# Optimization experiments

Hardware: AMD Instinct MI355X
Metric: run time of the kernel (lower is better)

Reference implementation:

```python
import jax, jax.numpy as jnp
import numpy as np


def lstm(x, W, U, b):
    """Keras LSTM with activation='relu', recurrent_activation='sigmoid'.
    x: [B, S, E]; W: [E, 4u]; U: [u, 4u]; b: [4u]. Gate order i,f,c,o.
    Returns (all hidden states [B,S,u], last hidden [B,u])."""
    B = x.shape[0]
    u = U.shape[0]
    h0 = jnp.zeros((B, u), x.dtype)
    c0 = jnp.zeros((B, u), x.dtype)

    def step(carry, xt):
        h, c = carry
        z = xt @ W + h @ U + b
        i, f, g, o = jnp.split(z, 4, axis=-1)
        i = jax.nn.sigmoid(i)
        f = jax.nn.sigmoid(f)
        g = jax.nn.relu(g)          # candidate activation = relu
        o = jax.nn.sigmoid(o)
        c = f * c + i * g
        h = o * jax.nn.relu(c)      # output activation = relu
        return (h, c), h

    (hT, _), hs = jax.lax.scan(step, (h0, c0), jnp.swapaxes(x, 0, 1))
    return jnp.swapaxes(hs, 0, 1), hT


def setup_inputs() -> dict:
    key = jax.random.key(0)
    ks = iter(jax.random.split(key, 64))

    def W(*s):
        return jax.random.normal(next(ks), s, jnp.float32) * 0.05

    V = 32000
    inp = {
        "t": jax.random.randint(next(ks), (8, 16, 64), 0, V, jnp.int32),
        "p": jax.random.randint(next(ks), (8, 16, 512), 0, V, jnp.int32),
        "emb_t": W(V, 128),
        "emb_p": W(V, 256),
        # title LSTMs: 128 (return_seq) -> 64
        "tl0_W": W(128, 512), "tl0_U": W(128, 512), "tl0_b": jnp.zeros((512,), jnp.float32),
        "tl1_W": W(128, 256), "tl1_U": W(64, 256),  "tl1_b": jnp.zeros((256,), jnp.float32),
        # title dense: 128 relu, 64 relu, 32 linear
        "td0_W": W(64, 128),  "td0_b": jnp.zeros((128,), jnp.float32),
        "td1_W": W(128, 64),  "td1_b": jnp.zeros((64,), jnp.float32),
        "td2_W": W(64, 32),   "td2_b": jnp.zeros((32,), jnp.float32),
        # parag LSTMs: 256 (rs) -> 128 (rs) -> 64
        "pl0_W": W(256, 1024), "pl0_U": W(256, 1024), "pl0_b": jnp.zeros((1024,), jnp.float32),
        "pl1_W": W(256, 512),  "pl1_U": W(128, 512),  "pl1_b": jnp.zeros((512,), jnp.float32),
        "pl2_W": W(128, 256),  "pl2_U": W(64, 256),   "pl2_b": jnp.zeros((256,), jnp.float32),
        # parag dense: 128 relu, 64 relu, 32 linear
        "pd0_W": W(64, 128),  "pd0_b": jnp.zeros((128,), jnp.float32),
        "pd1_W": W(128, 64),  "pd1_b": jnp.zeros((64,), jnp.float32),
        "pd2_W": W(64, 32),   "pd2_b": jnp.zeros((32,), jnp.float32),
        # head: 256 relu, 128 relu, 64 relu, 32 sigmoid
        "L0_W": W(64, 256),  "L0_b": jnp.zeros((256,), jnp.float32),
        "L1_W": W(256, 128), "L1_b": jnp.zeros((128,), jnp.float32),
        "L2_W": W(128, 64),  "L2_b": jnp.zeros((64,), jnp.float32),
        "L3_W": W(64, 32),   "L3_b": jnp.zeros((32,), jnp.float32),
    }
    return inp


def reference(t, p, emb_t, emb_p,
              tl0_W, tl0_U, tl0_b, tl1_W, tl1_U, tl1_b,
              td0_W, td0_b, td1_W, td1_b, td2_W, td2_b,
              pl0_W, pl0_U, pl0_b, pl1_W, pl1_U, pl1_b, pl2_W, pl2_U, pl2_b,
              pd0_W, pd0_b, pd1_W, pd1_b, pd2_W, pd2_b,
              L0_W, L0_b, L1_W, L1_b, L2_W, L2_b, L3_W, L3_b):
    B, N, St = t.shape
    Sp = p.shape[2]

    # The original loops over B and map_fn over a singleton axis; the math is
    # identical to running the stacks on a flattened [B*N] recurrent batch.
    xt = emb_t[t.reshape(B * N, St)]              # [BN, St, 128]
    xt, _ = lstm(xt, tl0_W, tl0_U, tl0_b)         # [BN, St, 128]
    _, ht = lstm(xt, tl1_W, tl1_U, tl1_b)         # [BN, 64]
    ht = jax.nn.relu(ht @ td0_W + td0_b)
    ht = jax.nn.relu(ht @ td1_W + td1_b)
    ht = ht @ td2_W + td2_b                       # [BN, 32] (no activation)

    xp = emb_p[p.reshape(B * N, Sp)]              # [BN, Sp, 256]
    xp, _ = lstm(xp, pl0_W, pl0_U, pl0_b)
    xp, _ = lstm(xp, pl1_W, pl1_U, pl1_b)
    _, hp = lstm(xp, pl2_W, pl2_U, pl2_b)         # [BN, 64]
    hp = jax.nn.relu(hp @ pd0_W + pd0_b)
    hp = jax.nn.relu(hp @ pd1_W + pd1_b)
    hp = hp @ pd2_W + pd2_b                       # [BN, 32]

    feat = jnp.concatenate([ht, hp], axis=-1).reshape(B, N, 64)
    x = feat.mean(axis=1)                         # reduce_mean over axis=-2 (N)
    x = jax.nn.relu(x @ L0_W + L0_b)
    x = jax.nn.relu(x @ L1_W + L1_b)
    x = jax.nn.relu(x @ L2_W + L2_b)
    x = jax.nn.sigmoid(x @ L3_W + L3_b)           # [B, 32]
    return x
```

## Files before the change

### kernel.cpp

```cpp
#include <hip/hip_runtime.h>
#include <hip/hip_fp16.h>

typedef _Float16 f16;
typedef _Float16 f16x8 __attribute__((ext_vector_type(8)));
typedef float    f32x4 __attribute__((ext_vector_type(4)));
typedef unsigned short ushort;
typedef unsigned int uint;
typedef unsigned long long u64;

__device__ __forceinline__ float sigm(float x) { return 1.f / (1.f + __expf(-x)); }
__device__ __forceinline__ float reluf(float x) { return x > 0.f ? x : 0.f; }
__device__ __forceinline__ float h2f(ushort u) { return (float)__builtin_bit_cast(f16, u); }
__device__ __forceinline__ ushort f2h(float v) { return __builtin_bit_cast(ushort, (f16)v); }

#define LDRLX(p)    __hip_atomic_load((p), __ATOMIC_RELAXED, __HIP_MEMORY_SCOPE_AGENT)
#define STRLX(p, v) __hip_atomic_store((p), (v), __ATOMIC_RELAXED, __HIP_MEMORY_SCOPE_AGENT)
#define MFMA16(a, b, c) __builtin_amdgcn_mfma_f32_16x16x32_f16((a), (b), (c), 0, 0, 0)
#define LBAR() do { asm volatile("s_waitcnt lgkmcnt(0)" ::: "memory"); \
                    __builtin_amdgcn_s_barrier(); } while (0)

__device__ __forceinline__ void poll_all(uint* p, uint need, bool act) {
  bool done = !act;
  while (true) {
    if (!done) done = (LDRLX(p) >= need);
    if (__all((int)done)) break;
    __builtin_amdgcn_s_sleep(1);
  }
}

__device__ __forceinline__ u64 ldr64(const u64* p) {
  return __hip_atomic_load(p, __ATOMIC_RELAXED, __HIP_MEMORY_SCOPE_AGENT);
}
__device__ __forceinline__ void str64(u64* p, u64 v) {
  __hip_atomic_store(p, v, __ATOMIC_RELAXED, __HIP_MEMORY_SCOPE_AGENT);
}

template <int NR>
__device__ __forceinline__ void poll_recs(const u64* const (&ra)[NR],
                                          const uint (&nd)[NR], u64 (&rv)[NR]) {
  bool ok[NR];
#pragma unroll
  for (int i = 0; i < NR; i++) ok[i] = (nd[i] == 0u);
  while (true) {
    bool all = true;
#pragma unroll
    for (int i = 0; i < NR; i++) if (!ok[i]) rv[i] = ldr64(ra[i]);
#pragma unroll
    for (int i = 0; i < NR; i++) if (!ok[i]) ok[i] = ((uint)(rv[i] >> 32) >= nd[i]);
#pragma unroll
    for (int i = 0; i < NR; i++) all &= ok[i];
    if (all) return;
    __builtin_amdgcn_s_sleep(1);
  }
}

template <int KF>
__global__ void pack_bsw(const float* __restrict__ B, f16* __restrict__ dst, int N) {
  int id = blockIdx.x * 256 + threadIdx.x;
  int total = KF * 32 * N;
  if (id >= total) return;
  int j  = id & 7;
  int L  = (id >> 3) & 63;
  int r  = id >> 9;
  int kf = r & (KF - 1);
  int c  = r / KF;
  int k  = kf * 32 + ((L >> 4) * 8) + j;
  int n  = c * 16 + (L & 15);
  dst[id] = (f16)B[k * N + n];
}

template <int Sx, int K, int KF, int N, int NC, int MODE>
__global__ __launch_bounds__(256) void gemm_xw(const int* __restrict__ tok,
                                               const float* __restrict__ emb,
                                               const f16* __restrict__ Bsw,
                                               const float* __restrict__ bias,
                                               f16* __restrict__ X) {
  __shared__ int tokLds[64];
  __shared__ f16x8 bLds[8 * 64];
  const int tid = threadIdx.x;
  const int blk = blockIdx.x;
  const int g  = (MODE == 0) ? (blk >> 7) : (blk >> 4);
  const int t0 = (MODE == 0) ? ((blk & 127) * 4) : ((blk & 15) * 4);
  if (tid < 64) {
    int wv = tid >> 4, rho = tid & 15;
    tokLds[tid] = tok[(g * 16 + rho) * Sx + t0 + wv];
  }
  __syncthreads();
  const int wave = tid >> 6, lane = tid & 63;
  const int quad = lane >> 4, l16 = lane & 15;

  f16x8 a[KF];
  {
    const float* arow = emb + (long)tokLds[wave * 16 + l16] * K + quad * 8;
#pragma unroll
    for (int kf = 0; kf < KF; kf++) {
      float4 v0 = *(const float4*)(arow + kf * 32);
      float4 v1 = *(const float4*)(arow + kf * 32 + 4);
      f16x8 tv;
      tv[0] = (f16)v0.x; tv[1] = (f16)v0.y; tv[2] = (f16)v0.z; tv[3] = (f16)v0.w;
      tv[4] = (f16)v1.x; tv[5] = (f16)v1.y; tv[6] = (f16)v1.z; tv[7] = (f16)v1.w;
      a[kf] = tv;
    }
  }
  const int t = t0 + wave;
  const f16x8* Bfrag = (const f16x8*)Bsw;
  for (int c = 0; c < NC; c++) {
    for (int i = tid; i < KF * 64; i += 256) bLds[i] = Bfrag[c * KF * 64 + i];
    __syncthreads();
    f32x4 acc = {0.f, 0.f, 0.f, 0.f};
#pragma unroll
    for (int kf = 0; kf < KF; kf++)
      acc = MFMA16(a[kf], bLds[kf * 64 + lane], acc);
    const int col = c * 16 + l16;
    const float bc = bias[col];
    uint2 pk;
    pk.x = (uint)f2h(acc[0] + bc) | ((uint)f2h(acc[1] + bc) << 16);
    pk.y = (uint)f2h(acc[2] + bc) | ((uint)f2h(acc[3] + bc) << 16);
    size_t base;
    if (MODE == 0) {
      int gm = col >> 8, u = col & 255;
      base = (((size_t)(g * 512 + t) * 4 + gm) * 4096) + u * 16 + quad * 4;
    } else {
      int gm = col >> 7, u = col & 127;
      base = (((size_t)(g * 64 + t) * 4 + gm) * 2048) + u * 16 + quad * 4;
    }
    *(uint2*)(X + base) = pk;
    __syncthreads();
  }
}

struct RP {
  const f16 *xp2, *xt2;
  const f16 *U0f, *W1f, *U1f, *W2f, *U2f, *U0tf, *W1tf, *U1tf;
  const float *pl1_b, *pl2_b, *tl1_b;
  const float *pd0W, *pd0b, *pd1W, *pd1b, *pd2W, *pd2b;
  const float *td0W, *td0b, *td1W, *td1b, *td2W, *td2b;
  u64 *h0r, *h1r, *h0tr;
  uint *cnt;
  float* feat;
};

__global__ __launch_bounds__(256, 1) void recur_pipe(RP A) {
  __shared__ __align__(16) char smem[147968];
  const int tid = threadIdx.x;
  const int w = tid >> 6, lane = tid & 63;
  const int quad = lane >> 4, l16 = lane & 15;
  const int blk = blockIdx.x;
  const int role = blk >> 3, g = blk & 7;
  uint* mytag = A.cnt + (role * 8 + g) * 16;

  if (role < 4) {
    const int bb = role;
    f16* wlds = (f16*)smem;
    f16* hb   = (f16*)(smem + 131072);
    {
      const uint4* U0q = (const uint4*)A.U0f;
      uint4* wq = (uint4*)wlds;
      for (int idx = tid; idx < 8192; idx += 256) {
        int gm = idx >> 11, r = idx & 2047, wv = r >> 9, kf = (r >> 6) & 7, ln = r & 63;
        wq[idx] = U0q[((gm * 16 + 4 * bb + wv) * 8 + kf) * 64 + ln];
      }
    }
    for (int idx = tid; idx < 4224; idx += 256) hb[idx] = (f16)0.f;
    float c0[4] = {0.f, 0.f, 0.f, 0.f};
    u64* ringg = A.h0r + (size_t)g * 16384;
    int pp[3]; { int q = 0; for (int p = 0; p < 4; p++) if (p != bb) pp[q++] = p; }
    const uint2* xq2 = (const uint2*)A.xp2;
    const f16x8* wv8 = (const f16x8*)wlds;
    const int myu = 64 * bb + 16 * w + l16;
    const int ulq = 16 * ((tid >> 4) & 3) + (tid & 15);
    const int qd  = tid >> 6;
    uint* bpp = A.cnt;
    if (lane < 4) bpp = A.cnt + ((4 + lane) * 8 + g) * 16;
    __syncthreads();

    for (int t = 0; t < 512; t++) {
      uint2 xv[4];
      {
        size_t xb = ((size_t)(g * 512 + t) * 4) * 1024 + (size_t)myu * 4 + quad;
#pragma unroll
        for (int gm = 0; gm < 4; gm++) xv[gm] = xq2[xb + (size_t)gm * 1024];
      }
      {
        bool act = (lane < 4) && (t > 0) && ((t & 3) == 0);
        uint need = t > 4 ? (uint)(t - 4) : 0u;
        poll_all(bpp, need, act);
      }
      {
        const u64* slotb = ringg + (size_t)((t + 7) & 7) * 2048;
        const u64* ra[6]; uint nd[6]; u64 rv[6];
#pragma unroll
        for (int q = 0; q < 3; q++) {
          const u64* rb = slotb + pp[q] * 512 + 2 * tid;
          ra[q * 2] = rb; ra[q * 2 + 1] = rb + 1;
          nd[q * 2] = nd[q * 2 + 1] = (t > 0) ? (uint)t : 0u;
        }
        poll_recs<6>(ra, nd, rv);
        if (t > 0) {
          f16* dst = hb + (t & 1) * 4224;
#pragma unroll
          for (int q = 0; q < 3; q++)
#pragma unroll
            for (int j = 0; j < 2; j++) {
              uint pay = (uint)rv[q * 2 + j];
              int r0 = qd * 4 + 2 * j;
              dst[r0 * 264 + pp[q] * 64 + ulq]       = __builtin_bit_cast(f16, (ushort)pay);
              dst[(r0 + 1) * 264 + pp[q] * 64 + ulq] = __builtin_bit_cast(f16, (ushort)(pay >> 16));
            }
        }
      }
      LBAR();
      f16x8 af[8];
#pragma unroll
      for (int kf = 0; kf < 8; kf++)
        af[kf] = *(const f16x8*)&hb[(t & 1) * 4224 + l16 * 264 + kf * 32 + quad * 8];
      f32x4 z[4];
#pragma unroll
      for (int gm = 0; gm < 4; gm++) {
        f32x4 zz = {0.f, 0.f, 0.f, 0.f};
#pragma unroll
        for (int kf = 0; kf < 8; kf++)
          zz = MFMA16(af[kf], wv8[((gm * 4 + w) * 8 + kf) * 64 + lane], zz);
        z[gm] = zz;
      }
      u64 xs[4];
#pragma unroll
      for (int gm = 0; gm < 4; gm++) xs[gm] = ((u64)xv[gm].y << 32) | xv[gm].x;
      ushort hs[4];
      f16* wbuf = hb + ((t + 1) & 1) * 4224;
#pragma unroll
      for (int r = 0; r < 4; r++) {
        float gi = sigm(z[0][r] + h2f((ushort)(xs[0] >> (16 * r))));
        float ff = sigm(z[1][r] + h2f((ushort)(xs[1] >> (16 * r))));
        float gg = reluf(z[2][r] + h2f((ushort)(xs[2] >> (16 * r))));
        float oo = sigm(z[3][r] + h2f((ushort)(xs[3] >> (16 * r))));
        c0[r] = ff * c0[r] + gi * gg;
        hs[r] = f2h(oo * reluf(c0[r]));
        wbuf[(quad * 4 + r) * 264 + myu] = __builtin_bit_cast(f16, hs[r]);
      }
      {
        u64 tg = ((u64)(uint)(t + 1)) << 32;
        u64* wb = ringg + (size_t)(t & 7) * 2048 + bb * 512 +
                  quad * 128 + w * 32 + l16 * 2;
        str64(wb,     tg | (u64)((uint)hs[0] | ((uint)hs[1] << 16)));
        str64(wb + 1, tg | (u64)((uint)hs[2] | ((uint)hs[3] << 16)));
      }
    }
  } else if (role < 8) {
    const int bn = role - 4;
    f16* wlds = (f16*)smem;
    f16* h0c  = (f16*)(smem + 98304);
    f16* h1b  = (f16*)(smem + 106752);
    float* zL = (float*)(smem + 115456);
    {
      const uint4* W1q = (const uint4*)A.W1f;
      const uint4* U1q = (const uint4*)A.U1f;
      uint4* wq = (uint4*)wlds;
      for (int idx = tid; idx < 4096; idx += 256) {
        int gm = idx >> 10, r = idx & 1023, j2 = r >> 9, kf = (r >> 6) & 7, ln = r & 63;
        wq[idx] = W1q[((gm * 8 + bn * 2 + j2) * 8 + kf) * 64 + ln];
      }
      for (int idx = tid; idx < 2048; idx += 256) {
        int gm = idx >> 9, r = idx & 511, j2 = r >> 8, kf = (r >> 6) & 3, ln = r & 63;
        wq[4096 + idx] = U1q[((gm * 8 + bn * 2 + j2) * 4 + kf) * 64 + ln];
      }
    }
    for (int idx = tid; idx < 2176; idx += 256) h1b[idx] = (f16)0.f;
    float c1[2] = {0.f, 0.f};
    float bth[4];
    { int un = tid & 31; for (int gm = 0; gm < 4; gm++) bth[gm] = A.pl1_b[gm * 128 + 32 * bn + un]; }
    u64* h0rg = A.h0r + (size_t)g * 16384;
    u64* h1rg = A.h1r + (size_t)g * 8192;
    int pp[3]; { int q = 0; for (int p = 0; p < 4; p++) if (p != bn) pp[q++] = p; }
    const f16x8* wv8 = (const f16x8*)wlds;
    uint* bpp = A.cnt + (8 * 8 + g) * 16;
    __syncthreads();

    for (int t = 0; t < 512; t++) {
      {
        bool act = (lane == 0) && ((t & 3) == 0);
        uint need = t > 4 ? (uint)(t - 4) : 0u;
        poll_all(bpp, need, act);
      }
      const u64* ra[11]; uint nd[11]; u64 rv[11];
      {
        const u64* s0b = h0rg + (size_t)(t & 7) * 2048;
#pragma unroll
        for (int e = 0; e < 8; e++) { ra[e] = s0b + tid + 256 * e; nd[e] = (uint)(t + 1); }
        const u64* s1b = h1rg + (size_t)((t + 7) & 7) * 1024;
#pragma unroll
        for (int q = 0; q < 3; q++) { ra[8 + q] = s1b + pp[q] * 256 + tid; nd[8 + q] = (t > 0) ? (uint)t : 0u; }
      }
      poll_recs<11>(ra, nd, rv);
      {
#pragma unroll
        for (int e = 0; e < 8; e++) {
          int idx = tid + 256 * e;
          int bbq = idx >> 9, r = idx & 511;
          int jj = r & 1, l16c = (r >> 1) & 15, wc = (r >> 5) & 3, qdc = (r >> 7) & 3;
          int col = bbq * 64 + 16 * wc + l16c;
          int r0 = qdc * 4 + 2 * jj;
          uint pay = (uint)rv[e];
          h0c[r0 * 264 + col]       = __builtin_bit_cast(f16, (ushort)pay);
          h0c[(r0 + 1) * 264 + col] = __builtin_bit_cast(f16, (ushort)(pay >> 16));
        }
        if (t > 0) {
          f16* dst = h1b + (t & 1) * 2176;
          int sqc = tid >> 5, unc = tid & 31;
#pragma unroll
          for (int q = 0; q < 3; q++) {
            uint pay = (uint)rv[8 + q];
            dst[sqc * 136 + pp[q] * 32 + unc]       = __builtin_bit_cast(f16, (ushort)pay);
            dst[(sqc + 8) * 136 + pp[q] * 32 + unc] = __builtin_bit_cast(f16, (ushort)(pay >> 16));
          }
        }
      }
      LBAR();
      if (tid == 0) STRLX(mytag, (uint)(t + 1));
      f16x8 af0[8], af1[4];
#pragma unroll
      for (int kf = 0; kf < 8; kf++)
        af0[kf] = *(const f16x8*)&h0c[l16 * 264 + kf * 32 + quad * 8];
#pragma unroll
      for (int kf = 0; kf < 4; kf++)
        af1[kf] = *(const f16x8*)&h1b[(t & 1) * 2176 + l16 * 136 + kf * 32 + quad * 8];
#pragma unroll
      for (int j2 = 0; j2 < 2; j2++) {
        f32x4 zz = {0.f, 0.f, 0.f, 0.f};
#pragma unroll
        for (int kf = 0; kf < 8; kf++)
          zz = MFMA16(af0[kf], wv8[((w * 2 + j2) * 8 + kf) * 64 + lane], zz);
#pragma unroll
        for (int kf = 0; kf < 4; kf++)
          zz = MFMA16(af1[kf], wv8[4096 + ((w * 2 + j2) * 4 + kf) * 64 + lane], zz);
#pragma unroll
        for (int r = 0; r < 4; r++)
          zL[(quad * 4 + r) * 132 + w * 32 + j2 * 16 + l16] = zz[r];
      }
      LBAR();
      {
        int sq = tid >> 5, un = tid & 31;
        f16* dst = h1b + ((t + 1) & 1) * 2176;
        ushort hh[2];
#pragma unroll
        for (int e = 0; e < 2; e++) {
          int s = sq + 8 * e;
          float gi = sigm(zL[s * 132 + un] + bth[0]);
          float ff = sigm(zL[s * 132 + 32 + un] + bth[1]);
          float gg = reluf(zL[s * 132 + 64 + un] + bth[2]);
          float oo = sigm(zL[s * 132 + 96 + un] + bth[3]);
          c1[e] = ff * c1[e] + gi * gg;
          float hv = oo * reluf(c1[e]);
          hh[e] = f2h(hv);
          dst[s * 136 + 32 * bn + un] = __builtin_bit_cast(f16, hh[e]);
        }
        u64 tg = ((u64)(uint)(t + 1)) << 32;
        str64(h1rg + (size_t)(t & 7) * 1024 + bn * 256 + tid,
              tg | (u64)((uint)hh[0] | ((uint)hh[1] << 16)));
      }
      LBAR();
    }
  } else if (role == 8) {
    f16* wlds = (f16*)smem;
    f16* h1c  = (f16*)(smem + 98304);
    f16* h2db = (f16*)(smem + 107008);
    {
      const uint4* W2q = (const uint4*)A.W2f;
      const uint4* U2q = (const uint4*)A.U2f;
      uint4* wq = (uint4*)wlds;
      for (int idx = tid; idx < 4096; idx += 256) wq[idx] = W2q[idx];
      for (int idx = tid; idx < 2048; idx += 256) wq[4096 + idx] = U2q[idx];
    }
    for (int idx = tid; idx < 1152; idx += 256) h2db[idx] = (f16)0.f;
    float c2[4] = {0.f, 0.f, 0.f, 0.f};
    float b2[4];
#pragma unroll
    for (int gm = 0; gm < 4; gm++) b2[gm] = A.pl2_b[gm * 64 + 16 * w + l16];
    u64* h1rg = A.h1r + (size_t)g * 8192;
    const f16x8* wv8 = (const f16x8*)wlds;
    __syncthreads();

    for (int t = 0; t < 512; t++) {
      const u64* ra[4]; uint nd[4]; u64 rv[4];
      {
        const u64* s1b = h1rg + (size_t)(t & 7) * 1024;
#pragma unroll
        for (int e = 0; e < 4; e++) { ra[e] = s1b + tid + 256 * e; nd[e] = (uint)(t + 1); }
      }
      poll_recs<4>(ra, nd, rv);
      {
        f16* dst = h1c + (t & 1) * 2176;
#pragma unroll
        for (int e = 0; e < 4; e++) {
          int idx = tid + 256 * e;
          int bq = idx >> 8, r = idx & 255;
          int sqc = r >> 5, unc = r & 31;
          uint pay = (uint)rv[e];
          dst[sqc * 136 + bq * 32 + unc]       = __builtin_bit_cast(f16, (ushort)pay);
          dst[(sqc + 8) * 136 + bq * 32 + unc] = __builtin_bit_cast(f16, (ushort)(pay >> 16));
        }
      }
      LBAR();
      if (tid == 0) STRLX(mytag, (uint)(t + 1));
      f16x8 af0[4], af1[2];
#pragma unroll
      for (int kf = 0; kf < 4; kf++)
        af0[kf] = *(const f16x8*)&h1c[(t & 1) * 2176 + l16 * 136 + kf * 32 + quad * 8];
#pragma unroll
      for (int kf = 0; kf < 2; kf++)
        af1[kf] = *(const f16x8*)&h2db[(t & 1) * 1152 + l16 * 72 + kf * 32 + quad * 8];
      f32x4 z[4];
#pragma unroll
      for (int gm = 0; gm < 4; gm++) {
        f32x4 zz = {0.f, 0.f, 0.f, 0.f};
#pragma unroll
        for (int kf = 0; kf < 4; kf++)
          zz = MFMA16(af0[kf], wv8[((gm * 4 + w) * 4 + kf) * 64 + lane], zz);
#pragma unroll
        for (int kf = 0; kf < 2; kf++)
          zz = MFMA16(af1[kf], wv8[4096 + ((gm * 4 + w) * 2 + kf) * 64 + lane], zz);
        z[gm] = zz;
      }
#pragma unroll
      for (int r = 0; r < 4; r++) {
        float gi = sigm(z[0][r] + b2[0]);
        float ff = sigm(z[1][r] + b2[1]);
        float gg = reluf(z[2][r] + b2[2]);
        float oo = sigm(z[3][r] + b2[3]);
        c2[r] = ff * c2[r] + gi * gg;
        h2db[((t + 1) & 1) * 1152 + (quad * 4 + r) * 72 + 16 * w + l16] = (f16)(oo * reluf(c2[r]));
      }
    }
    __syncthreads();
    float* zmA = (float*)smem;
    float* zmB = (float*)(smem + 8448);
    const f16* hf = h2db;
#pragma unroll 1
    for (int e = 0; e < 8; e++) {
      const int idx = tid + 256 * e, sq = idx >> 7, j = idx & 127;
      float a = A.pd0b[j];
      for (int k = 0; k < 64; k++) a += (float)hf[sq * 72 + k] * A.pd0W[k * 128 + j];
      zmA[sq * 132 + j] = reluf(a);
    }
    __syncthreads();
#pragma unroll 1
    for (int e = 0; e < 4; e++) {
      const int idx = tid + 256 * e, sq = idx >> 6, j = idx & 63;
      float a = A.pd1b[j];
      for (int k = 0; k < 128; k++) a += zmA[sq * 132 + k] * A.pd1W[k * 64 + j];
      zmB[sq * 68 + j] = reluf(a);
    }
    __syncthreads();
#pragma unroll 1
    for (int e = 0; e < 2; e++) {
      const int idx = tid + 256 * e, sq = idx >> 5, j = idx & 31;
      float a = A.pd2b[j];
      for (int k = 0; k < 64; k++) a += zmB[sq * 68 + k] * A.pd2W[k * 32 + j];
      A.feat[(g * 16 + sq) * 64 + 32 + j] = a;
    }
  } else if (role < 11) {
    const int bb = role - 9;
    f16* wlds = (f16*)smem;
    f16* hb   = (f16*)(smem + 65536);
    {
      const uint4* U0tq = (const uint4*)A.U0tf;
      uint4* wq = (uint4*)wlds;
      for (int idx = tid; idx < 4096; idx += 256) {
        int gm = idx >> 10, r = idx & 1023, wv = r >> 8, kf = (r >> 6) & 3, ln = r & 63;
        wq[idx] = U0tq[((gm * 8 + 4 * bb + wv) * 4 + kf) * 64 + ln];
      }
    }
    for (int idx = tid; idx < 2176; idx += 256) hb[idx] = (f16)0.f;
    float c0[4] = {0.f, 0.f, 0.f, 0.f};
    u64* ringg = A.h0tr + (size_t)g * 8192;
    const uint2* xq2 = (const uint2*)A.xt2;
    const f16x8* wv8 = (const f16x8*)wlds;
    const int myu = 64 * bb + 16 * w + l16;
    const int pbb = bb ^ 1;
    uint* bpp = A.cnt + (11 * 8 + g) * 16;
    __syncthreads();

    for (int t = 0; t < 64; t++) {
      uint2 xv[4];
      {
        size_t xb = ((size_t)(g * 64 + t) * 4) * 512 + (size_t)myu * 4 + quad;
#pragma unroll
        for (int gm = 0; gm < 4; gm++) xv[gm] = xq2[xb + (size_t)gm * 512];
      }
      {
        bool act = (lane == 0) && (t > 0) && ((t & 3) == 0);
        uint need = t > 4 ? (uint)(t - 4) : 0u;
        poll_all(bpp, need, act);
      }
      {
        const u64* ra[2]; uint nd[2]; u64 rv[2];
        const u64* rb = ringg + (size_t)((t + 7) & 7) * 1024 + pbb * 512 + 2 * tid;
        ra[0] = rb; ra[1] = rb + 1;
        nd[0] = nd[1] = (t > 0) ? (uint)t : 0u;
        poll_recs<2>(ra, nd, rv);
        if (t > 0) {
          f16* dst = hb + (t & 1) * 2176;
          const int ul = tid >> 2;
#pragma unroll
          for (int j = 0; j < 2; j++) {
            uint pay = (uint)rv[j];
            int r0 = ((tid & 3) * 2 + j) * 2;
            dst[r0 * 136 + pbb * 64 + ul]       = __builtin_bit_cast(f16, (ushort)pay);
            dst[(r0 + 1) * 136 + pbb * 64 + ul] = __builtin_bit_cast(f16, (ushort)(pay >> 16));
          }
        }
      }
      LBAR();
      f16x8 af[4];
#pragma unroll
      for (int kf = 0; kf < 4; kf++)
        af[kf] = *(const f16x8*)&hb[(t & 1) * 2176 + l16 * 136 + kf * 32 + quad * 8];
      f32x4 z[4];
#pragma unroll
      for (int gm = 0; gm < 4; gm++) {
        f32x4 zz = {0.f, 0.f, 0.f, 0.f};
#pragma unroll
        for (int kf = 0; kf < 4; kf++)
          zz = MFMA16(af[kf], wv8[((gm * 4 + w) * 4 + kf) * 64 + lane], zz);
        z[gm] = zz;
      }
      u64 xs[4];
#pragma unroll
      for (int gm = 0; gm < 4; gm++) xs[gm] = ((u64)xv[gm].y << 32) | xv[gm].x;
      ushort hs[4];
      f16* wbuf = hb + ((t + 1) & 1) * 2176;
#pragma unroll
      for (int r = 0; r < 4; r++) {
        float gi = sigm(z[0][r] + h2f((ushort)(xs[0] >> (16 * r))));
        float ff = sigm(z[1][r] + h2f((ushort)(xs[1] >> (16 * r))));
        float gg = reluf(z[2][r] + h2f((ushort)(xs[2] >> (16 * r))));
        float oo = sigm(z[3][r] + h2f((ushort)(xs[3] >> (16 * r))));
        c0[r] = ff * c0[r] + gi * gg;
        hs[r] = f2h(oo * reluf(c0[r]));
        wbuf[(quad * 4 + r) * 136 + myu] = __builtin_bit_cast(f16, hs[r]);
      }
      {
        u64 tg = ((u64)(uint)(t + 1)) << 32;
        u64* wb = ringg + (size_t)(t & 7) * 1024 + bb * 512 + (16 * w + l16) * 8 + quad * 2;
        str64(wb,     tg | (u64)((uint)hs[0] | ((uint)hs[1] << 16)));
        str64(wb + 1, tg | (u64)((uint)hs[2] | ((uint)hs[3] << 16)));
      }
    }
  } else {
    f16* wlds = (f16*)smem;
    f16* h0tc = (f16*)(smem + 98304);
    f16* h1db = (f16*)(smem + 107008);
    {
      const uint4* W1tq = (const uint4*)A.W1tf;
      const uint4* U1tq = (const uint4*)A.U1tf;
      uint4* wq = (uint4*)wlds;
      for (int idx = tid; idx < 4096; idx += 256) wq[idx] = W1tq[idx];
      for (int idx = tid; idx < 2048; idx += 256) wq[4096 + idx] = U1tq[idx];
    }
    for (int idx = tid; idx < 1152; idx += 256) h1db[idx] = (f16)0.f;
    float c1[4] = {0.f, 0.f, 0.f, 0.f};
    float bt[4];
#pragma unroll
    for (int gm = 0; gm < 4; gm++) bt[gm] = A.tl1_b[gm * 64 + 16 * w + l16];
    u64* ringg = A.h0tr + (size_t)g * 8192;
    const f16x8* wv8 = (const f16x8*)wlds;
    __syncthreads();

    for (int t = 0; t < 64; t++) {
      const u64* ra[4]; uint nd[4]; u64 rv[4];
      {
        const u64* base = ringg + (size_t)(t & 7) * 1024;
#pragma unroll
        for (int e = 0; e < 4; e++) { ra[e] = base + tid + 256 * e; nd[e] = (uint)(t + 1); }
      }
      poll_recs<4>(ra, nd, rv);
      {
        f16* dst = h0tc + (t & 1) * 2176;
#pragma unroll
        for (int e = 0; e < 4; e++) {
          int idx = tid + 256 * e;
          int q = idx >> 9, rr = idx & 511, uls = rr >> 3, rp = rr & 7;
          uint pay = (uint)rv[e];
          dst[(2 * rp) * 136 + q * 64 + uls]     = __builtin_bit_cast(f16, (ushort)pay);
          dst[(2 * rp + 1) * 136 + q * 64 + uls] = __builtin_bit_cast(f16, (ushort)(pay >> 16));
        }
      }
      LBAR();
      if (tid == 0) STRLX(mytag, (uint)(t + 1));
      f16x8 af0[4], af1[2];
#pragma unroll
      for (int kf = 0; kf < 4; kf++)
        af0[kf] = *(const f16x8*)&h0tc[(t & 1) * 2176 + l16 * 136 + kf * 32 + quad * 8];
#pragma unroll
      for (int kf = 0; kf < 2; kf++)
        af1[kf] = *(const f16x8*)&h1db[(t & 1) * 1152 + l16 * 72 + kf * 32 + quad * 8];
      f32x4 z[4];
#pragma unroll
      for (int gm = 0; gm < 4; gm++) {
        f32x4 zz = {0.f, 0.f, 0.f, 0.f};
#pragma unroll
        for (int kf = 0; kf < 4; kf++)
          zz = MFMA16(af0[kf], wv8[((gm * 4 + w) * 4 + kf) * 64 + lane], zz);
#pragma unroll
        for (int kf = 0; kf < 2; kf++)
          zz = MFMA16(af1[kf], wv8[4096 + ((gm * 4 + w) * 2 + kf) * 64 + lane], zz);
        z[gm] = zz;
      }
#pragma unroll
      for (int r = 0; r < 4; r++) {
        float gi = sigm(z[0][r] + bt[0]);
        float ff = sigm(z[1][r] + bt[1]);
        float gg = reluf(z[2][r] + bt[2]);
        float oo = sigm(z[3][r] + bt[3]);
        c1[r] = ff * c1[r] + gi * gg;
        h1db[((t + 1) & 1) * 1152 + (quad * 4 + r) * 72 + 16 * w + l16] = (f16)(oo * reluf(c1[r]));
      }
    }
    __syncthreads();
    float* zmA = (float*)smem;
    float* zmB = (float*)(smem + 8448);
    const f16* hf = h1db;
#pragma unroll 1
    for (int e = 0; e < 8; e++) {
      const int idx = tid + 256 * e, sq = idx >> 7, j = idx & 127;
      float a = A.td0b[j];
      for (int k = 0; k < 64; k++) a += (float)hf[sq * 72 + k] * A.td0W[k * 128 + j];
      zmA[sq * 132 + j] = reluf(a);
    }
    __syncthreads();
#pragma unroll 1
    for (int e = 0; e < 4; e++) {
      const int idx = tid + 256 * e, sq = idx >> 6, j = idx & 63;
      float a = A.td1b[j];
      for (int k = 0; k < 128; k++) a += zmA[sq * 132 + k] * A.td1W[k * 64 + j];
      zmB[sq * 68 + j] = reluf(a);
    }
    __syncthreads();
#pragma unroll 1
    for (int e = 0; e < 2; e++) {
      const int idx = tid + 256 * e, sq = idx >> 5, j = idx & 31;
      float a = A.td2b[j];
      for (int k = 0; k < 64; k++) a += zmB[sq * 68 + k] * A.td2W[k * 32 + j];
      A.feat[(g * 16 + sq) * 64 + j] = a;
    }
  }
}

__global__ __launch_bounds__(256) void head_kernel(const float* __restrict__ feat,
    const float* __restrict__ L0W, const float* __restrict__ L0b,
    const float* __restrict__ L1W, const float* __restrict__ L1b,
    const float* __restrict__ L2W, const float* __restrict__ L2b,
    const float* __restrict__ L3W, const float* __restrict__ L3b,
    float* __restrict__ out) {
  __shared__ float xb[512];
  __shared__ float y0[2048];
  __shared__ float y1[1024];
  __shared__ float y2[512];
  const int tid = threadIdx.x;
  for (int idx = tid; idx < 512; idx += 256) {
    int b = idx >> 6, d = idx & 63;
    float s = 0.f;
    for (int n = 0; n < 16; n++) s += feat[(b * 16 + n) * 64 + d];
    xb[idx] = s * (1.f / 16.f);
  }
  __syncthreads();
  for (int idx = tid; idx < 2048; idx += 256) {
    int b = idx >> 8, j = idx & 255;
    float a = L0b[j];
    for (int k = 0; k < 64; k++) a += xb[b * 64 + k] * L0W[k * 256 + j];
    y0[idx] = reluf(a);
  }
  __syncthreads();
  for (int idx = tid; idx < 1024; idx += 256) {
    int b = idx >> 7, j = idx & 127;
    float a = L1b[j];
    for (int k = 0; k < 256; k++) a += y0[b * 256 + k] * L1W[k * 128 + j];
    y1[idx] = reluf(a);
  }
  __syncthreads();
  for (int idx = tid; idx < 512; idx += 256) {
    int b = idx >> 6, j = idx & 63;
    float a = L2b[j];
    for (int k = 0; k < 128; k++) a += y1[b * 128 + k] * L2W[k * 64 + j];
    y2[idx] = reluf(a);
  }
  __syncthreads();
  {
    int b = tid >> 5, j = tid & 31;
    float a = L3b[j];
    for (int k = 0; k < 64; k++) a += y2[b * 64 + k] * L3W[k * 32 + j];
    out[b * 32 + j] = 1.f / (1.f + __expf(-a));
  }
}

extern "C" void kernel_launch(void* const* d_in, const int* in_sizes, int n_in,
                              void* d_out, int out_size, void* d_ws, size_t ws_size,
                              hipStream_t stream) {
  const int*   t_tok = (const int*)d_in[0];
  const int*   p_tok = (const int*)d_in[1];
  const float* emb_t = (const float*)d_in[2];
  const float* emb_p = (const float*)d_in[3];
  const float* tl0_W = (const float*)d_in[4];
  const float* tl0_U = (const float*)d_in[5];
  const float* tl0_b = (const float*)d_in[6];
  const float* tl1_W = (const float*)d_in[7];
  const float* tl1_U = (const float*)d_in[8];
  const float* tl1_b = (const float*)d_in[9];
  const float* td0_W = (const float*)d_in[10];
  const float* td0_b = (const float*)d_in[11];
  const float* td1_W = (const float*)d_in[12];
  const float* td1_b = (const float*)d_in[13];
  const float* td2_W = (const float*)d_in[14];
  const float* td2_b = (const float*)d_in[15];
  const float* pl0_W = (const float*)d_in[16];
  const float* pl0_U = (const float*)d_in[17];
  const float* pl0_b = (const float*)d_in[18];
  const float* pl1_W = (const float*)d_in[19];
  const float* pl1_U = (const float*)d_in[20];
  const float* pl1_b = (const float*)d_in[21];
  const float* pl2_W = (const float*)d_in[22];
  const float* pl2_U = (const float*)d_in[23];
  const float* pl2_b = (const float*)d_in[24];
  const float* pd0_W = (const float*)d_in[25];
  const float* pd0_b = (const float*)d_in[26];
  const float* pd1_W = (const float*)d_in[27];
  const float* pd1_b = (const float*)d_in[28];
  const float* pd2_W = (const float*)d_in[29];
  const float* pd2_b = (const float*)d_in[30];
  const float* L0_W  = (const float*)d_in[31];
  const float* L0_b  = (const float*)d_in[32];
  const float* L1_W  = (const float*)d_in[33];
  const float* L1_b  = (const float*)d_in[34];
  const float* L2_W  = (const float*)d_in[35];
  const float* L2_b  = (const float*)d_in[36];
  const float* L3_W  = (const float*)d_in[37];
  const float* L3_b  = (const float*)d_in[38];

  char* ws = (char*)d_ws;
  size_t off = 0;
  auto alloc = [&](size_t bytes) {
    void* ptr = ws + off;
    off += (bytes + 255) & ~(size_t)255;
    return ptr;
  };
  f16* xp2  = (f16*)alloc((size_t)8 * 512 * 4 * 4096 * 2);
  f16* xt2  = (f16*)alloc((size_t)8 * 64 * 4 * 2048 * 2);
  f16* Bp   = (f16*)alloc((size_t)256 * 1024 * 2);
  f16* Bt   = (f16*)alloc((size_t)128 * 512 * 2);
  f16* U0f  = (f16*)alloc((size_t)256 * 1024 * 2);
  f16* W1f  = (f16*)alloc((size_t)256 * 512 * 2);
  f16* U1f  = (f16*)alloc((size_t)128 * 512 * 2);
  f16* W2f  = (f16*)alloc((size_t)128 * 256 * 2);
  f16* U2f  = (f16*)alloc((size_t)64 * 256 * 2);
  f16* U0tf = (f16*)alloc((size_t)128 * 512 * 2);
  f16* W1tf = (f16*)alloc((size_t)128 * 256 * 2);
  f16* U1tf = (f16*)alloc((size_t)64 * 256 * 2);
  size_t ringoff = off;
  u64* h0r  = (u64*)alloc((size_t)8 * 16384 * 8);
  u64* h1r  = (u64*)alloc((size_t)8 * 8192 * 8);
  u64* h0tr = (u64*)alloc((size_t)8 * 8192 * 8);
  uint* cnt = (uint*)alloc((size_t)96 * 16 * 4);
  size_t ringlen = off - ringoff;
  float* feat = (float*)alloc((size_t)128 * 64 * 4);

  hipMemsetAsync(ws + ringoff, 0, ringlen, stream);

  pack_bsw<8><<<1024, 256, 0, stream>>>(pl0_W, Bp, 1024);
  pack_bsw<4><<<256, 256, 0, stream>>>(tl0_W, Bt, 512);
  pack_bsw<8><<<1024, 256, 0, stream>>>(pl0_U, U0f, 1024);
  pack_bsw<8><<<512, 256, 0, stream>>>(pl1_W, W1f, 512);
  pack_bsw<4><<<256, 256, 0, stream>>>(pl1_U, U1f, 512);
  pack_bsw<4><<<128, 256, 0, stream>>>(pl2_W, W2f, 256);
  pack_bsw<2><<<64, 256, 0, stream>>>(pl2_U, U2f, 256);
  pack_bsw<4><<<256, 256, 0, stream>>>(tl0_U, U0tf, 512);
  pack_bsw<4><<<128, 256, 0, stream>>>(tl1_W, W1tf, 256);
  pack_bsw<2><<<64, 256, 0, stream>>>(tl1_U, U1tf, 256);
  gemm_xw<512, 256, 8, 1024, 64, 0><<<1024, 256, 0, stream>>>(p_tok, emb_p, Bp, pl0_b, xp2);
  gemm_xw<64, 128, 4, 512, 32, 1><<<128, 256, 0, stream>>>(t_tok, emb_t, Bt, tl0_b, xt2);

  RP ra;
  ra.xp2 = xp2; ra.xt2 = xt2;
  ra.U0f = U0f; ra.W1f = W1f; ra.U1f = U1f; ra.W2f = W2f; ra.U2f = U2f;
  ra.U0tf = U0tf; ra.W1tf = W1tf; ra.U1tf = U1tf;
  ra.pl1_b = pl1_b; ra.pl2_b = pl2_b; ra.tl1_b = tl1_b;
  ra.pd0W = pd0_W; ra.pd0b = pd0_b; ra.pd1W = pd1_W; ra.pd1b = pd1_b;
  ra.pd2W = pd2_W; ra.pd2b = pd2_b;
  ra.td0W = td0_W; ra.td0b = td0_b; ra.td1W = td1_W; ra.td1b = td1_b;
  ra.td2W = td2_W; ra.td2b = td2_b;
  ra.h0r = h0r; ra.h1r = h1r; ra.h0tr = h0tr; ra.cnt = cnt;
  ra.feat = feat;
  recur_pipe<<<96, 256, 0, stream>>>(ra);

  head_kernel<<<1, 256, 0, stream>>>(feat, L0_W, L0_b, L1_W, L1_b, L2_W, L2_b,
                                     L3_W, L3_b, (float*)d_out);
}
```

Baseline: 1.455 ms.

## Fuse input-projection GEMM into the persistent recurrent kernel via flagged worker blocks

Moves the embedding-gather and input-projection GEMMs out of their own launches and into 160 extra worker blocks of the persistent recurrent kernel. Workers publish per-(group, 4-step chunk) ready flags, and the recurrent layer-0 blocks poll those flags before loading the x-projection. This lets the sequential recurrence start while later timesteps are still being projected, hiding GEMM time behind the recurrence. It relies on all 256 blocks being co-resident to avoid deadlock, and adds flag polling and atomic 64-bit loads and stores for the projected inputs.

```diff
diff --git a/kernel.cpp b/kernel.cpp
--- a/kernel.cpp
+++ b/kernel.cpp
@@ -69,18 +69,29 @@
   dst[id] = (f16)B[k * N + n];
 }
 
+struct RP {
+  const int *t_tok, *p_tok;
+  const float *emb_t, *emb_p;
+  const f16 *Bp, *Bt;
+  const float *tl0_b, *pl0_b;
+  f16 *xp2, *xt2;
+  const f16 *U0f, *W1f, *U1f, *W2f, *U2f, *U0tf, *W1tf, *U1tf;
+  const float *pl1_b, *pl2_b, *tl1_b;
+  const float *pd0W, *pd0b, *pd1W, *pd1b, *pd2W, *pd2b;
+  const float *td0W, *td0b, *td1W, *td1b, *td2W, *td2b;
+  u64 *h0r, *h1r, *h0tr;
+  uint *cnt, *xfl, *tfl;
+  float* feat;
+};
+
 template <int Sx, int K, int KF, int N, int NC, int MODE>
-__global__ __launch_bounds__(256) void gemm_xw(const int* __restrict__ tok,
-                                               const float* __restrict__ emb,
-                                               const f16* __restrict__ Bsw,
-                                               const float* __restrict__ bias,
-                                               f16* __restrict__ X) {
-  __shared__ int tokLds[64];
-  __shared__ f16x8 bLds[8 * 64];
+__device__ __forceinline__ void gemm_tile(int g, int t0,
+    const int* __restrict__ tok, const float* __restrict__ emb,
+    const f16* __restrict__ Bsw, const float* __restrict__ bias,
+    u64* __restrict__ X, char* smem) {
+  int* tokLds = (int*)smem;
+  f16x8* bLds = (f16x8*)(smem + 1024);
   const int tid = threadIdx.x;
-  const int blk = blockIdx.x;
-  const int g  = (MODE == 0) ? (blk >> 7) : (blk >> 4);
-  const int t0 = (MODE == 0) ? ((blk & 127) * 4) : ((blk & 15) * 4);
   if (tid < 64) {
     int wv = tid >> 4, rho = tid & 15;
     tokLds[tid] = tok[(g * 16 + rho) * Sx + t0 + wv];
@@ -88,7 +99,6 @@
   __syncthreads();
   const int wave = tid >> 6, lane = tid & 63;
   const int quad = lane >> 4, l16 = lane & 15;
-
   f16x8 a[KF];
   {
     const float* arow = emb + (long)tokLds[wave * 16 + l16] * K + quad * 8;
@@ -105,6 +115,7 @@
   const int t = t0 + wave;
   const f16x8* Bfrag = (const f16x8*)Bsw;
   for (int c = 0; c < NC; c++) {
+    __syncthreads();
     for (int i = tid; i < KF * 64; i += 256) bLds[i] = Bfrag[c * KF * 64 + i];
     __syncthreads();
     f32x4 acc = {0.f, 0.f, 0.f, 0.f};
@@ -113,39 +124,46 @@
       acc = MFMA16(a[kf], bLds[kf * 64 + lane], acc);
     const int col = c * 16 + l16;
     const float bc = bias[col];
-    uint2 pk;
-    pk.x = (uint)f2h(acc[0] + bc) | ((uint)f2h(acc[1] + bc) << 16);
-    pk.y = (uint)f2h(acc[2] + bc) | ((uint)f2h(acc[3] + bc) << 16);
-    size_t base;
+    uint lo = (uint)f2h(acc[0] + bc) | ((uint)f2h(acc[1] + bc) << 16);
+    uint hi = (uint)f2h(acc[2] + bc) | ((uint)f2h(acc[3] + bc) << 16);
+    u64 pv = (u64)lo | ((u64)hi << 32);
+    size_t b64;
     if (MODE == 0) {
       int gm = col >> 8, u = col & 255;
-      base = (((size_t)(g * 512 + t) * 4 + gm) * 4096) + u * 16 + quad * 4;
+      b64 = (((size_t)(g * 512 + t) * 4 + gm) * 1024) + u * 4 + quad;
     } else {
       int gm = col >> 7, u = col & 127;
-      base = (((size_t)(g * 64 + t) * 4 + gm) * 2048) + u * 16 + quad * 4;
-    }
-    *(uint2*)(X + base) = pk;
-    __syncthreads();
-  }
-}
-
-struct RP {
-  const f16 *xp2, *xt2;
-  const f16 *U0f, *W1f, *U1f, *W2f, *U2f, *U0tf, *W1tf, *U1tf;
-  const float *pl1_b, *pl2_b, *tl1_b;
-  const float *pd0W, *pd0b, *pd1W, *pd1b, *pd2W, *pd2b;
-  const float *td0W, *td0b, *td1W, *td1b, *td2W, *td2b;
-  u64 *h0r, *h1r, *h0tr;
-  uint *cnt;
-  float* feat;
-};
-
-__global__ __launch_bounds__(256, 1) void recur_pipe(RP A) {
+      b64 = (((size_t)(g * 64 + t) * 4 + gm) * 512) + u * 4 + quad;
+    }
+    str64(X + b64, pv);
+  }
+  __syncthreads();
+}
+
+__device__ void worker_body(const RP& A, int wid, char* smem) {
+  const int tid = threadIdx.x;
+  for (int tile = wid; tile < 1152; tile += 160) {
+    if (tile < 128) {
+      int tch = tile >> 3, g = tile & 7;
+      gemm_tile<64, 128, 4, 512, 32, 1>(g, tch * 4, A.t_tok, A.emb_t, A.Bt,
+                                        A.tl0_b, (u64*)A.xt2, smem);
+      if (tid == 0) STRLX(A.tfl + g * 16 + tch, 1u);
+    } else {
+      int m0 = tile - 128, tch = m0 >> 3, g = m0 & 7;
+      gemm_tile<512, 256, 8, 1024, 64, 0>(g, tch * 4, A.p_tok, A.emb_p, A.Bp,
+                                          A.pl0_b, (u64*)A.xp2, smem);
+      if (tid == 0) STRLX(A.xfl + g * 128 + tch, 1u);
+    }
+  }
+}
+
+__global__ __launch_bounds__(256, 1) void fused(RP A) {
   __shared__ __align__(16) char smem[147968];
+  const int blk = blockIdx.x;
+  if (blk >= 96) { worker_body(A, blk - 96, smem); return; }
   const int tid = threadIdx.x;
   const int w = tid >> 6, lane = tid & 63;
   const int quad = lane >> 4, l16 = lane & 15;
-  const int blk = blockIdx.x;
   const int role = blk >> 3, g = blk & 7;
   uint* mytag = A.cnt + (role * 8 + g) * 16;
 
@@ -164,34 +182,36 @@
     for (int idx = tid; idx < 4224; idx += 256) hb[idx] = (f16)0.f;
     float c0[4] = {0.f, 0.f, 0.f, 0.f};
     u64* ringg = A.h0r + (size_t)g * 16384;
-    int pp[3]; { int q = 0; for (int p = 0; p < 4; p++) if (p != bb) pp[q++] = p; }
-    const uint2* xq2 = (const uint2*)A.xp2;
+    int pp3[3]; { int q = 0; for (int p = 0; p < 4; p++) if (p != bb) pp3[q++] = p; }
+    const u64* xq2 = (const u64*)A.xp2;
     const f16x8* wv8 = (const f16x8*)wlds;
     const int myu = 64 * bb + 16 * w + l16;
     const int ulq = 16 * ((tid >> 4) & 3) + (tid & 15);
     const int qd  = tid >> 6;
     uint* bpp = A.cnt;
     if (lane < 4) bpp = A.cnt + ((4 + lane) * 8 + g) * 16;
+    uint* xflg = A.xfl + g * 128;
     __syncthreads();
 
     for (int t = 0; t < 512; t++) {
-      uint2 xv[4];
+      {
+        uint* pp = bpp; uint need = 0; bool act = false;
+        if (lane < 4) { act = (t > 0) && ((t & 3) == 0); need = t > 4 ? (uint)(t - 4) : 0u; }
+        else if (lane == 4) { act = ((t & 3) == 0); need = 1u; pp = xflg + (t >> 2); }
+        poll_all(pp, need, act);
+      }
+      u64 xs[4];
       {
         size_t xb = ((size_t)(g * 512 + t) * 4) * 1024 + (size_t)myu * 4 + quad;
 #pragma unroll
-        for (int gm = 0; gm < 4; gm++) xv[gm] = xq2[xb + (size_t)gm * 1024];
-      }
-      {
-        bool act = (lane < 4) && (t > 0) && ((t & 3) == 0);
-        uint need = t > 4 ? (uint)(t - 4) : 0u;
-        poll_all(bpp, need, act);
+        for (int gm = 0; gm < 4; gm++) xs[gm] = ldr64(xq2 + xb + (size_t)gm * 1024);
       }
       {
         const u64* slotb = ringg + (size_t)((t + 7) & 7) * 2048;
         const u64* ra[6]; uint nd[6]; u64 rv[6];
 #pragma unroll
         for (int q = 0; q < 3; q++) {
-          const u64* rb = slotb + pp[q] * 512 + 2 * tid;
+          const u64* rb = slotb + pp3[q] * 512 + 2 * tid;
           ra[q * 2] = rb; ra[q * 2 + 1] = rb + 1;
           nd[q * 2] = nd[q * 2 + 1] = (t > 0) ? (uint)t : 0u;
         }
@@ -204,8 +224,8 @@
             for (int j = 0; j < 2; j++) {
               uint pay = (uint)rv[q * 2 + j];
               int r0 = qd * 4 + 2 * j;
-              dst[r0 * 264 + pp[q] * 64 + ulq]       = __builtin_bit_cast(f16, (ushort)pay);
-              dst[(r0 + 1) * 264 + pp[q] * 64 + ulq] = __builtin_bit_cast(f16, (ushort)(pay >> 16));
+              dst[r0 * 264 + pp3[q] * 64 + ulq]       = __builtin_bit_cast(f16, (ushort)pay);
+              dst[(r0 + 1) * 264 + pp3[q] * 64 + ulq] = __builtin_bit_cast(f16, (ushort)(pay >> 16));
             }
         }
       }
@@ -223,9 +243,6 @@
           zz = MFMA16(af[kf], wv8[((gm * 4 + w) * 8 + kf) * 64 + lane], zz);
         z[gm] = zz;
       }
-      u64 xs[4];
-#pragma unroll
-      for (int gm = 0; gm < 4; gm++) xs[gm] = ((u64)xv[gm].y << 32) | xv[gm].x;
       ushort hs[4];
       f16* wbuf = hb + ((t + 1) & 1) * 4224;
 #pragma unroll
@@ -271,7 +288,7 @@
     { int un = tid & 31; for (int gm = 0; gm < 4; gm++) bth[gm] = A.pl1_b[gm * 128 + 32 * bn + un]; }
     u64* h0rg = A.h0r + (size_t)g * 16384;
     u64* h1rg = A.h1r + (size_t)g * 8192;
-    int pp[3]; { int q = 0; for (int p = 0; p < 4; p++) if (p != bn) pp[q++] = p; }
+    int pp3[3]; { int q = 0; for (int p = 0; p < 4; p++) if (p != bn) pp3[q++] = p; }
     const f16x8* wv8 = (const f16x8*)wlds;
     uint* bpp = A.cnt + (8 * 8 + g) * 16;
     __syncthreads();
@@ -289,7 +306,7 @@
         for (int e = 0; e < 8; e++) { ra[e] = s0b + tid + 256 * e; nd[e] = (uint)(t + 1); }
         const u64* s1b = h1rg + (size_t)((t + 7) & 7) * 1024;
 #pragma unroll
-        for (int q = 0; q < 3; q++) { ra[8 + q] = s1b + pp[q] * 256 + tid; nd[8 + q] = (t > 0) ? (uint)t : 0u; }
+        for (int q = 0; q < 3; q++) { ra[8 + q] = s1b + pp3[q] * 256 + tid; nd[8 + q] = (t > 0) ? (uint)t : 0u; }
       }
       poll_recs<11>(ra, nd, rv);
       {
@@ -310,8 +327,8 @@
 #pragma unroll
           for (int q = 0; q < 3; q++) {
             uint pay = (uint)rv[8 + q];
-            dst[sqc * 136 + pp[q] * 32 + unc]       = __builtin_bit_cast(f16, (ushort)pay);
-            dst[(sqc + 8) * 136 + pp[q] * 32 + unc] = __builtin_bit_cast(f16, (ushort)(pay >> 16));
+            dst[sqc * 136 + pp3[q] * 32 + unc]       = __builtin_bit_cast(f16, (ushort)pay);
+            dst[(sqc + 8) * 136 + pp3[q] * 32 + unc] = __builtin_bit_cast(f16, (ushort)(pay >> 16));
           }
         }
       }
@@ -473,24 +490,26 @@
     for (int idx = tid; idx < 2176; idx += 256) hb[idx] = (f16)0.f;
     float c0[4] = {0.f, 0.f, 0.f, 0.f};
     u64* ringg = A.h0tr + (size_t)g * 8192;
-    const uint2* xq2 = (const uint2*)A.xt2;
+    const u64* xtq = (const u64*)A.xt2;
     const f16x8* wv8 = (const f16x8*)wlds;
     const int myu = 64 * bb + 16 * w + l16;
     const int pbb = bb ^ 1;
     uint* bpp = A.cnt + (11 * 8 + g) * 16;
+    uint* tflg = A.tfl + g * 16;
     __syncthreads();
 
     for (int t = 0; t < 64; t++) {
-      uint2 xv[4];
+      {
+        uint* pp = bpp; uint need = 0; bool act = false;
+        if (lane == 0) { act = (t > 0) && ((t & 3) == 0); need = t > 4 ? (uint)(t - 4) : 0u; }
+        else if (lane == 1) { act = ((t & 3) == 0); need = 1u; pp = tflg + (t >> 2); }
+        poll_all(pp, need, act);
+      }
+      u64 xs[4];
       {
         size_t xb = ((size_t)(g * 64 + t) * 4) * 512 + (size_t)myu * 4 + quad;
 #pragma unroll
-        for (int gm = 0; gm < 4; gm++) xv[gm] = xq2[xb + (size_t)gm * 512];
-      }
-      {
-        bool act = (lane == 0) && (t > 0) && ((t & 3) == 0);
-        uint need = t > 4 ? (uint)(t - 4) : 0u;
-        poll_all(bpp, need, act);
+        for (int gm = 0; gm < 4; gm++) xs[gm] = ldr64(xtq + xb + (size_t)gm * 512);
       }
       {
         const u64* ra[2]; uint nd[2]; u64 rv[2];
@@ -524,9 +543,6 @@
           zz = MFMA16(af[kf], wv8[((gm * 4 + w) * 4 + kf) * 64 + lane], zz);
         z[gm] = zz;
       }
-      u64 xs[4];
-#pragma unroll
-      for (int gm = 0; gm < 4; gm++) xs[gm] = ((u64)xv[gm].y << 32) | xv[gm].x;
       ushort hs[4];
       f16* wbuf = hb + ((t + 1) & 1) * 2176;
 #pragma unroll
@@ -760,13 +776,15 @@
   u64* h1r  = (u64*)alloc((size_t)8 * 8192 * 8);
   u64* h0tr = (u64*)alloc((size_t)8 * 8192 * 8);
   uint* cnt = (uint*)alloc((size_t)96 * 16 * 4);
+  uint* xfl = (uint*)alloc((size_t)8 * 128 * 4);
+  uint* tfl = (uint*)alloc((size_t)8 * 16 * 4);
   size_t ringlen = off - ringoff;
   float* feat = (float*)alloc((size_t)128 * 64 * 4);
 
   hipMemsetAsync(ws + ringoff, 0, ringlen, stream);
 
+  pack_bsw<4><<<256, 256, 0, stream>>>(tl0_W, Bt, 512);
   pack_bsw<8><<<1024, 256, 0, stream>>>(pl0_W, Bp, 1024);
-  pack_bsw<4><<<256, 256, 0, stream>>>(tl0_W, Bt, 512);
   pack_bsw<8><<<1024, 256, 0, stream>>>(pl0_U, U0f, 1024);
   pack_bsw<8><<<512, 256, 0, stream>>>(pl1_W, W1f, 512);
   pack_bsw<4><<<256, 256, 0, stream>>>(pl1_U, U1f, 512);
@@ -775,10 +793,10 @@
   pack_bsw<4><<<256, 256, 0, stream>>>(tl0_U, U0tf, 512);
   pack_bsw<4><<<128, 256, 0, stream>>>(tl1_W, W1tf, 256);
   pack_bsw<2><<<64, 256, 0, stream>>>(tl1_U, U1tf, 256);
-  gemm_xw<512, 256, 8, 1024, 64, 0><<<1024, 256, 0, stream>>>(p_tok, emb_p, Bp, pl0_b, xp2);
-  gemm_xw<64, 128, 4, 512, 32, 1><<<128, 256, 0, stream>>>(t_tok, emb_t, Bt, tl0_b, xt2);
 
   RP ra;
+  ra.t_tok = t_tok; ra.p_tok = p_tok; ra.emb_t = emb_t; ra.emb_p = emb_p;
+  ra.Bp = Bp; ra.Bt = Bt; ra.tl0_b = tl0_b; ra.pl0_b = pl0_b;
   ra.xp2 = xp2; ra.xt2 = xt2;
   ra.U0f = U0f; ra.W1f = W1f; ra.U1f = U1f; ra.W2f = W2f; ra.U2f = U2f;
   ra.U0tf = U0tf; ra.W1tf = W1tf; ra.U1tf = U1tf;
@@ -787,9 +805,10 @@
   ra.pd2W = pd2_W; ra.pd2b = pd2_b;
   ra.td0W = td0_W; ra.td0b = td0_b; ra.td1W = td1_W; ra.td1b = td1_b;
   ra.td2W = td2_W; ra.td2b = td2_b;
-  ra.h0r = h0r; ra.h1r = h1r; ra.h0tr = h0tr; ra.cnt = cnt;
+  ra.h0r = h0r; ra.h1r = h1r; ra.h0tr = h0tr;
+  ra.cnt = cnt; ra.xfl = xfl; ra.tfl = tfl;
   ra.feat = feat;
-  recur_pipe<<<96, 256, 0, stream>>>(ra);
+  fused<<<256, 256, 0, stream>>>(ra);
 
   head_kernel<<<1, 256, 0, stream>>>(feat, L0_W, L0_b, L1_W, L1_b, L2_W, L2_b,
                                      L3_W, L3_b, (float*)d_out);
```

New measurement: 1.409 ms. -3.2%, faster.
